# Kernel tuning notes

Hardware: AMD Instinct MI355X
Metric: run time of the kernel (lower is better)

Reference implementation:

```python
import jax, jax.numpy as jnp
import numpy as np

TEMPERATURE = 0.07
EPS = 1e-12  # matches torch F.normalize default eps


def setup_inputs() -> dict:
    key = jax.random.key(0)
    k1, k2 = jax.random.split(key)
    features1 = jax.random.normal(k1, (16384, 512), dtype=jnp.float32)
    features2 = jax.random.normal(k2, (16384, 512), dtype=jnp.float32)
    return {"features1": features1, "features2": features2}


def _l2_normalize(x):
    # torch F.normalize: x / max(||x||, eps)
    norm = jnp.sqrt(jnp.sum(x * x, axis=1, keepdims=True))
    return x / jnp.maximum(norm, EPS)


def reference(features1, features2):
    f1 = _l2_normalize(features1)
    f2 = _l2_normalize(features2)
    # [N, N] similarity logits
    logits = jnp.einsum('nd,md->nm', f1, f2) / TEMPERATURE
    n = logits.shape[0]
    # cross-entropy with labels = arange(n): mean over rows of (logsumexp - diag logit)
    log_probs = jax.nn.log_softmax(logits, axis=1)
    diag = jnp.diagonal(log_probs)
    loss = -jnp.mean(diag)
    return loss
```

## Files before the change

kernel.cpp:

```cpp
#include <hip/hip_runtime.h>
#include <stdint.h>

#define NROWS 16384
#define KDIM  512
#define BM 256
#define BN 256
#define CT 2
#define NCHUNK 32
#define NPHASE 16
#define INV_T 14.285714285714286f
#define LOG2E 1.4426950408889634f
#define LN2   0.6931471805599453f

typedef __bf16 bf16x8 __attribute__((ext_vector_type(8)));
typedef float  f32x16 __attribute__((ext_vector_type(16)));
typedef unsigned short u16x8 __attribute__((ext_vector_type(8)));

__device__ __forceinline__ void gload_lds16(const void* gptr, void* lptr) {
    uint32_t loff = (uint32_t)(uintptr_t)lptr;
    loff = __builtin_amdgcn_readfirstlane(loff);
    __builtin_amdgcn_global_load_lds(
        (const uint32_t __attribute__((address_space(1)))*)(uintptr_t)gptr,
        (uint32_t __attribute__((address_space(3)))*)(uintptr_t)loff,
        16, 0, 0);
}


__global__ void k_norm(const float* __restrict__ X, char* __restrict__ Y, float scale) {
    const int row  = blockIdx.x * 4 + (threadIdx.x >> 6);
    const int lane = threadIdx.x & 63;
    const float* xr = X + (size_t)row * KDIM + lane * 8;
    float4 a = *(const float4*)xr;
    float4 b = *(const float4*)(xr + 4);
    float ss = a.x*a.x + a.y*a.y + a.z*a.z + a.w*a.w
             + b.x*b.x + b.y*b.y + b.z*b.z + b.w*b.w;
    #pragma unroll
    for (int off = 1; off < 64; off <<= 1) ss += __shfl_xor(ss, off);
    const float s = scale / fmaxf(sqrtf(ss), 1e-12f);
    __bf16 o[8];
    o[0] = (__bf16)(a.x * s); o[1] = (__bf16)(a.y * s);
    o[2] = (__bf16)(a.z * s); o[3] = (__bf16)(a.w * s);
    o[4] = (__bf16)(b.x * s); o[5] = (__bf16)(b.y * s);
    o[6] = (__bf16)(b.z * s); o[7] = (__bf16)(b.w * s);
    const int kh = lane >> 2, q = lane & 3;
    const size_t gr = ((size_t)(kh * 512 + (row >> 5)) * 2 + (q >> 1)) * 64
                    + ((q & 1) << 5) + (row & 31);
    *(u16x8*)(Y + gr * 16) = *(const u16x8*)o;
}

__global__ __launch_bounds__(512, 1) void k_gemm(const char* __restrict__ A,
                                                 const char* __restrict__ B,
                                                 float* __restrict__ S_part) {
    __shared__ __align__(16) char L[4 * 32768];
    __shared__ float rowsum[4][BM];

    const int tid  = threadIdx.x;
    const int lane = tid & 63;
    const int w    = tid >> 6;
    const int wr   = w >> 2, wc = w & 3;
    const int bid  = blockIdx.x;
    const int xcd  = bid & 7;
    const int idx  = bid >> 3;
    const int st   = idx >> 5;
    const int wsub = idx & 31;
    const int brow  = (st * 8 + (wsub >> 2)) * BM;
    const int chunk = xcd * 4 + (wsub & 3);

    const int lbyte = lane * 16;

#define STAGE(h_, s_) do {                                               \
        const char* ga_ = A + (size_t)((h_) * NROWS + brow) * 64 + tid * 16; \
        const char* gb_ = B + (size_t)((h_) * NROWS + bcol) * 64 + tid * 16; \
        char* la_ = L + (s_) * 32768 + tid * 16;                         \
        gload_lds16(ga_,        la_);                                    \
        gload_lds16(ga_ + 8192, la_ + 8192);                             \
        gload_lds16(gb_,        la_ + 16384);                            \
        gload_lds16(gb_ + 8192, la_ + 24576);                            \
    } while (0)

    float rowacc = 0.f;
    for (int ct = 0; ct < CT; ++ct) {
        const int bcol = (chunk * CT + ct) * BN;
        f32x16 acc[4][2] = {};

        STAGE(0, 0);
        STAGE(1, 1);
        asm volatile("s_waitcnt vmcnt(4)" ::: "memory");
        __builtin_amdgcn_s_barrier();
        __builtin_amdgcn_sched_barrier(0);

        #pragma unroll
        for (int h = 0; h < NPHASE; ++h) {
            if (h < NPHASE - 2) STAGE(h + 2, (h + 2) & 3);
            const char* sl = L + (h & 3) * 32768;
            bf16x8 af[4][2], bf[2][2];
            #pragma unroll
            for (int m = 0; m < 4; ++m)
                #pragma unroll
                for (int ks = 0; ks < 2; ++ks)
                    af[m][ks] = *(const bf16x8*)(sl + ((wr * 4 + m) * 2 + ks) * 1024 + lbyte);
            #pragma unroll
            for (int n = 0; n < 2; ++n)
                #pragma unroll
                for (int ks = 0; ks < 2; ++ks)
                    bf[n][ks] = *(const bf16x8*)(sl + 16384 + ((wc * 2 + n) * 2 + ks) * 1024 + lbyte);
            __builtin_amdgcn_s_setprio(1);
            #pragma unroll
            for (int m = 0; m < 4; ++m)
                #pragma unroll
                for (int n = 0; n < 2; ++n)
                    #pragma unroll
                    for (int ks = 0; ks < 2; ++ks)
                        acc[m][n] = __builtin_amdgcn_mfma_f32_32x32x16_bf16(
                            af[m][ks], bf[n][ks], acc[m][n], 0, 0, 0);
            __builtin_amdgcn_s_setprio(0);
            if (h < NPHASE - 2)       asm volatile("s_waitcnt vmcnt(4)" ::: "memory");
            else if (h == NPHASE - 2) asm volatile("s_waitcnt vmcnt(0)" ::: "memory");
            __builtin_amdgcn_s_barrier();
            __builtin_amdgcn_sched_barrier(0);
        }

        #pragma unroll
        for (int m = 0; m < 4; ++m) {
            float rs[16];
            #pragma unroll
            for (int r = 0; r < 16; ++r)
                rs[r] = __builtin_amdgcn_exp2f(acc[m][0][r])
                      + __builtin_amdgcn_exp2f(acc[m][1][r]);
            #pragma unroll
            for (int off = 16; off >= 1; off >>= 1)
                #pragma unroll
                for (int r = 0; r < 16; ++r)
                    rs[r] += __shfl_xor(rs[r], off);
            if ((lane & 31) == 0) {
                const int rb = wr * 128 + m * 32 + (lane >> 5) * 4;
                #pragma unroll
                for (int r = 0; r < 16; ++r)
                    rowsum[wc][rb + (r & 3) + 8 * (r >> 2)] = rs[r];
            }
        }
        __syncthreads();
        if (tid < BM)
            rowacc += rowsum[0][tid] + rowsum[1][tid] + rowsum[2][tid] + rowsum[3][tid];
        __syncthreads();
    }
#undef STAGE
    if (tid < BM) S_part[(size_t)chunk * NROWS + brow + tid] = rowacc;
}

__global__ void k_diag(const char* __restrict__ A, const char* __restrict__ B,
                       float* __restrict__ diag) {
    const int row  = blockIdx.x * 4 + (threadIdx.x >> 6);
    const int lane = threadIdx.x & 63;
    const int kh = lane >> 2, q = lane & 3;
    const size_t gr = ((size_t)(kh * 512 + (row >> 5)) * 2 + (q >> 1)) * 64
                    + ((q & 1) << 5) + (row & 31);
    const bf16x8 va = *(const bf16x8*)(A + gr * 16);
    const bf16x8 vb = *(const bf16x8*)(B + gr * 16);
    float d = 0.f;
    #pragma unroll
    for (int i = 0; i < 8; ++i) d += (float)va[i] * (float)vb[i];
    #pragma unroll
    for (int off2 = 1; off2 < 64; off2 <<= 1) d += __shfl_xor(d, off2);
    if (lane == 0) diag[row] = d;
}

__global__ void k_loss(const float* __restrict__ S_part, const float* __restrict__ diag,
                       float* __restrict__ partial) {
    const int g = blockIdx.x * 256 + threadIdx.x;
    float S = 0.f;
    #pragma unroll
    for (int c = 0; c < NCHUNK; ++c) S += S_part[(size_t)c * NROWS + g];
    float v = logf(S) - diag[g] * LN2;
    __shared__ float wsum[4];
    #pragma unroll
    for (int off = 1; off < 64; off <<= 1) v += __shfl_xor(v, off);
    if ((threadIdx.x & 63) == 0) wsum[threadIdx.x >> 6] = v;
    __syncthreads();
    if (threadIdx.x == 0) partial[blockIdx.x] = wsum[0] + wsum[1] + wsum[2] + wsum[3];
}

__global__ void k_final(const float* __restrict__ partial, float* __restrict__ out) {
    float v = partial[threadIdx.x];
    #pragma unroll
    for (int off = 1; off < 64; off <<= 1) v += __shfl_xor(v, off);
    if (threadIdx.x == 0) out[0] = v * (1.0f / (float)NROWS);
}

extern "C" void kernel_launch(void* const* d_in, const int* in_sizes, int n_in,
                              void* d_out, int out_size, void* d_ws, size_t ws_size,
                              hipStream_t stream) {
    const float* f1 = (const float*)d_in[0];
    const float* f2 = (const float*)d_in[1];
    float* out = (float*)d_out;

    char* ws = (char*)d_ws;
    char*  f1p   = ws;
    char*  f2p   = ws + (16u << 20);
    float* S_part = (float*)(ws + (32u << 20));
    float* diag   = (float*)(ws + (34u << 20));
    float* part   = (float*)(ws + (34u << 20) + (1u << 16));

    k_norm<<<dim3(NROWS / 4), dim3(256), 0, stream>>>(f1, f1p, INV_T * LOG2E);
    k_norm<<<dim3(NROWS / 4), dim3(256), 0, stream>>>(f2, f2p, 1.0f);
    k_gemm<<<dim3((NROWS / BM) * NCHUNK), dim3(512), 0, stream>>>(f1p, f2p, S_part);
    k_diag<<<dim3(NROWS / 4), dim3(256), 0, stream>>>(f1p, f2p, diag);
    k_loss<<<dim3(NROWS / 256), dim3(256), 0, stream>>>(S_part, diag, part);
    k_final<<<dim3(1), dim3(64), 0, stream>>>(part, out);
}
```

Before: 395.2 us.

## Restructure GEMM into 64-wide K tiles with 16x16x32 MFMA and interleaved ping-pong schedule

Repacks the normalized bf16 operands into a new 64-wide K-tile layout and switches the GEMM from 32x32x16 to 16x16x32 MFMA, using 8x4 accumulator tiles per wave. The main loop becomes a two-buffer, 64KB-per-stage ping-pong that interleaves LDS fragment reads, global-to-LDS staging, and MFMA clusters, with barriers between each quarter. The aim is better overlap of memory traffic with matrix math and fewer phases per tile. It adds many more barriers and raises launch_bounds to 2 blocks per CU, although the LDS footprint (about 132KB) may still limit occupancy to one block.

```diff
diff --git a/kernel.cpp b/kernel.cpp
--- a/kernel.cpp
+++ b/kernel.cpp
@@ -7,13 +7,12 @@
 #define BN 256
 #define CT 2
 #define NCHUNK 32
-#define NPHASE 16
 #define INV_T 14.285714285714286f
 #define LOG2E 1.4426950408889634f
 #define LN2   0.6931471805599453f
 
 typedef __bf16 bf16x8 __attribute__((ext_vector_type(8)));
-typedef float  f32x16 __attribute__((ext_vector_type(16)));
+typedef float  f32x4  __attribute__((ext_vector_type(4)));
 typedef unsigned short u16x8 __attribute__((ext_vector_type(8)));
 
 __device__ __forceinline__ void gload_lds16(const void* gptr, void* lptr) {
@@ -42,17 +41,18 @@
     o[2] = (__bf16)(a.z * s); o[3] = (__bf16)(a.w * s);
     o[4] = (__bf16)(b.x * s); o[5] = (__bf16)(b.y * s);
     o[6] = (__bf16)(b.z * s); o[7] = (__bf16)(b.w * s);
-    const int kh = lane >> 2, q = lane & 3;
-    const size_t gr = ((size_t)(kh * 512 + (row >> 5)) * 2 + (q >> 1)) * 64
-                    + ((q & 1) << 5) + (row & 31);
+    const int kt = lane >> 3, ksub = (lane >> 2) & 1, oo = lane & 3;
+    const size_t gr = ((size_t)(kt * 64 + (row >> 8)) * 2048)
+                    + ((((row >> 4) & 15) * 2 + ksub) * 64) + oo * 16 + (row & 15);
     *(u16x8*)(Y + gr * 16) = *(const u16x8*)o;
 }
 
-__global__ __launch_bounds__(512, 1) void k_gemm(const char* __restrict__ A,
+__global__ __launch_bounds__(512, 2) void k_gemm(const char* __restrict__ A,
                                                  const char* __restrict__ B,
                                                  float* __restrict__ S_part) {
-    __shared__ __align__(16) char L[4 * 32768];
+    __shared__ __align__(16) char L[2 * 65536];
     __shared__ float rowsum[4][BM];
+    char* Lc = (char*)L;
 
     const int tid  = threadIdx.x;
     const int lane = tid & 63;
@@ -65,78 +65,108 @@
     const int wsub = idx & 31;
     const int brow  = (st * 8 + (wsub >> 2)) * BM;
     const int chunk = xcd * 4 + (wsub & 3);
-
-    const int lbyte = lane * 16;
-
-#define STAGE(h_, s_) do {                                               \
-        const char* ga_ = A + (size_t)((h_) * NROWS + brow) * 64 + tid * 16; \
-        const char* gb_ = B + (size_t)((h_) * NROWS + bcol) * 64 + tid * 16; \
-        char* la_ = L + (s_) * 32768 + tid * 16;                         \
-        gload_lds16(ga_,        la_);                                    \
-        gload_lds16(ga_ + 8192, la_ + 8192);                             \
-        gload_lds16(gb_,        la_ + 16384);                            \
-        gload_lds16(gb_ + 8192, la_ + 24576);                            \
+    const int rbA = brow >> 8;
+
+#define STG(P_, RB_, KT_, LB_) do {                                           \
+        const char* g_ = (P_) + ((size_t)((KT_) * 64 + (RB_)) * 32768) + tid * 16; \
+        char* l_ = Lc + (LB_) + tid * 16;                                     \
+        gload_lds16(g_,         l_);                                          \
+        gload_lds16(g_ +  8192, l_ +  8192);                                  \
+        gload_lds16(g_ + 16384, l_ + 16384);                                  \
+        gload_lds16(g_ + 24576, l_ + 24576);                                  \
+    } while (0)
+
+#define RD_A4(MLO_, BUFB_) do {                                               \
+        _Pragma("unroll") for (int m_ = 0; m_ < 4; ++m_)                      \
+        _Pragma("unroll") for (int ks_ = 0; ks_ < 2; ++ks_)                   \
+            a[m_][ks_] = *(const bf16x8*)(Lc + (BUFB_)                        \
+                + (((wr * 8 + (MLO_) + m_) * 2 + ks_) << 10) + (lane << 4));  \
+    } while (0)
+
+#define RD_B2(NLO_, BUFB_) do {                                               \
+        _Pragma("unroll") for (int n_ = 0; n_ < 2; ++n_)                      \
+        _Pragma("unroll") for (int ks_ = 0; ks_ < 2; ++ks_)                   \
+            b[n_][ks_] = *(const bf16x8*)(Lc + (BUFB_) + 32768                \
+                + (((wc * 4 + (NLO_) + n_) * 2 + ks_) << 10) + (lane << 4));  \
+    } while (0)
+
+#define MM8(MLO_, NLO_) do {                                                  \
+        __builtin_amdgcn_s_setprio(1);                                        \
+        _Pragma("unroll") for (int m_ = 0; m_ < 4; ++m_)                      \
+        _Pragma("unroll") for (int n_ = 0; n_ < 2; ++n_)                      \
+        _Pragma("unroll") for (int ks_ = 0; ks_ < 2; ++ks_)                   \
+            acc[(MLO_) + m_][(NLO_) + n_] =                                   \
+                __builtin_amdgcn_mfma_f32_16x16x32_bf16(                      \
+                    a[m_][ks_], b[n_][ks_], acc[(MLO_) + m_][(NLO_) + n_],    \
+                    0, 0, 0);                                                 \
+        __builtin_amdgcn_s_setprio(0);                                        \
+    } while (0)
+
+#define BAR_LGKM() do {                                                       \
+        __builtin_amdgcn_s_barrier();                                         \
+        asm volatile("s_waitcnt lgkmcnt(0)" ::: "memory");                    \
+        __builtin_amdgcn_sched_barrier(0);                                    \
     } while (0)
 
     float rowacc = 0.f;
     for (int ct = 0; ct < CT; ++ct) {
-        const int bcol = (chunk * CT + ct) * BN;
-        f32x16 acc[4][2] = {};
-
-        STAGE(0, 0);
-        STAGE(1, 1);
-        asm volatile("s_waitcnt vmcnt(4)" ::: "memory");
+        const int rbB = chunk * CT + ct;
+        f32x4 acc[8][4] = {};
+        bf16x8 a[4][2], b[2][2];
+
+        STG(A, rbA, 0, 0);
+        STG(B, rbB, 0, 32768);
+        STG(A, rbA, 1, 65536);
+        STG(B, rbB, 1, 98304);
+        asm volatile("s_waitcnt vmcnt(8)" ::: "memory");
         __builtin_amdgcn_s_barrier();
-        __builtin_amdgcn_sched_barrier(0);
 
         #pragma unroll
-        for (int h = 0; h < NPHASE; ++h) {
-            if (h < NPHASE - 2) STAGE(h + 2, (h + 2) & 3);
-            const char* sl = L + (h & 3) * 32768;
-            bf16x8 af[4][2], bf[2][2];
+        for (int i = 0; i < 4; ++i) {
+            RD_A4(0, 0); RD_B2(0, 0);
+            if (i > 0) STG(A, rbA, 2 * i + 1, 65536);
+            asm volatile("s_waitcnt lgkmcnt(8)" ::: "memory");
+            BAR_LGKM(); MM8(0, 0); __builtin_amdgcn_s_barrier();
+            RD_B2(2, 0);
+            if (i > 0) STG(B, rbB, 2 * i + 1, 98304);
+            BAR_LGKM(); MM8(0, 2); __builtin_amdgcn_s_barrier();
+            RD_A4(4, 0);
+            BAR_LGKM(); MM8(4, 2); __builtin_amdgcn_s_barrier();
+            RD_B2(0, 0);
+            asm volatile("s_waitcnt vmcnt(0)" ::: "memory");
+            BAR_LGKM(); MM8(4, 0); __builtin_amdgcn_s_barrier();
+            RD_A4(0, 65536); RD_B2(0, 65536);
+            if (i < 3) STG(A, rbA, 2 * i + 2, 0);
+            asm volatile("s_waitcnt lgkmcnt(8)" ::: "memory");
+            BAR_LGKM(); MM8(0, 0); __builtin_amdgcn_s_barrier();
+            RD_B2(2, 65536);
+            if (i < 3) STG(B, rbB, 2 * i + 2, 32768);
+            BAR_LGKM(); MM8(0, 2); __builtin_amdgcn_s_barrier();
+            RD_A4(4, 65536);
+            BAR_LGKM(); MM8(4, 2); __builtin_amdgcn_s_barrier();
+            RD_B2(0, 65536);
+            if (i < 3) asm volatile("s_waitcnt vmcnt(0)" ::: "memory");
+            BAR_LGKM(); MM8(4, 0); __builtin_amdgcn_s_barrier();
+        }
+
+        #pragma unroll
+        for (int m = 0; m < 8; ++m) {
+            float rs[4];
             #pragma unroll
-            for (int m = 0; m < 4; ++m)
+            for (int r = 0; r < 4; ++r)
+                rs[r] = __builtin_amdgcn_exp2f(acc[m][0][r])
+                      + __builtin_amdgcn_exp2f(acc[m][1][r])
+                      + __builtin_amdgcn_exp2f(acc[m][2][r])
+                      + __builtin_amdgcn_exp2f(acc[m][3][r]);
+            #pragma unroll
+            for (int off = 8; off >= 1; off >>= 1)
                 #pragma unroll
-                for (int ks = 0; ks < 2; ++ks)
-                    af[m][ks] = *(const bf16x8*)(sl + ((wr * 4 + m) * 2 + ks) * 1024 + lbyte);
-            #pragma unroll
-            for (int n = 0; n < 2; ++n)
+                for (int r = 0; r < 4; ++r)
+                    rs[r] += __shfl_xor(rs[r], off);
+            if ((lane & 15) == 0) {
                 #pragma unroll
-                for (int ks = 0; ks < 2; ++ks)
-                    bf[n][ks] = *(const bf16x8*)(sl + 16384 + ((wc * 2 + n) * 2 + ks) * 1024 + lbyte);
-            __builtin_amdgcn_s_setprio(1);
-            #pragma unroll
-            for (int m = 0; m < 4; ++m)
-                #pragma unroll
-                for (int n = 0; n < 2; ++n)
-                    #pragma unroll
-                    for (int ks = 0; ks < 2; ++ks)
-                        acc[m][n] = __builtin_amdgcn_mfma_f32_32x32x16_bf16(
-                            af[m][ks], bf[n][ks], acc[m][n], 0, 0, 0);
-            __builtin_amdgcn_s_setprio(0);
-            if (h < NPHASE - 2)       asm volatile("s_waitcnt vmcnt(4)" ::: "memory");
-            else if (h == NPHASE - 2) asm volatile("s_waitcnt vmcnt(0)" ::: "memory");
-            __builtin_amdgcn_s_barrier();
-            __builtin_amdgcn_sched_barrier(0);
-        }
-
-        #pragma unroll
-        for (int m = 0; m < 4; ++m) {
-            float rs[16];
-            #pragma unroll
-            for (int r = 0; r < 16; ++r)
-                rs[r] = __builtin_amdgcn_exp2f(acc[m][0][r])
-                      + __builtin_amdgcn_exp2f(acc[m][1][r]);
-            #pragma unroll
-            for (int off = 16; off >= 1; off >>= 1)
-                #pragma unroll
-                for (int r = 0; r < 16; ++r)
-                    rs[r] += __shfl_xor(rs[r], off);
-            if ((lane & 31) == 0) {
-                const int rb = wr * 128 + m * 32 + (lane >> 5) * 4;
-                #pragma unroll
-                for (int r = 0; r < 16; ++r)
-                    rowsum[wc][rb + (r & 3) + 8 * (r >> 2)] = rs[r];
+                for (int r = 0; r < 4; ++r)
+                    rowsum[wc][wr * 128 + m * 16 + (lane >> 4) * 4 + r] = rs[r];
             }
         }
         __syncthreads();
@@ -144,7 +174,11 @@
             rowacc += rowsum[0][tid] + rowsum[1][tid] + rowsum[2][tid] + rowsum[3][tid];
         __syncthreads();
     }
-#undef STAGE
+#undef STG
+#undef RD_A4
+#undef RD_B2
+#undef MM8
+#undef BAR_LGKM
     if (tid < BM) S_part[(size_t)chunk * NROWS + brow + tid] = rowacc;
 }
 
@@ -152,9 +186,9 @@
                        float* __restrict__ diag) {
     const int row  = blockIdx.x * 4 + (threadIdx.x >> 6);
     const int lane = threadIdx.x & 63;
-    const int kh = lane >> 2, q = lane & 3;
-    const size_t gr = ((size_t)(kh * 512 + (row >> 5)) * 2 + (q >> 1)) * 64
-                    + ((q & 1) << 5) + (row & 31);
+    const int kt = lane >> 3, ksub = (lane >> 2) & 1, oo = lane & 3;
+    const size_t gr = ((size_t)(kt * 64 + (row >> 8)) * 2048)
+                    + ((((row >> 4) & 15) * 2 + ksub) * 64) + oo * 16 + (row & 15);
     const bf16x8 va = *(const bf16x8*)(A + gr * 16);
     const bf16x8 vb = *(const bf16x8*)(B + gr * 16);
     float d = 0.f;
```

Result: slower. 476.1 us (+20.5%).
